# Kernel tuning notes

Measured on AMD Instinct MI355X. Metric: run time of the kernel, lower is better.

The kernel has to match this reference:

```python
import jax, jax.numpy as jnp
import numpy as np


def setup_inputs() -> dict:
    key = jax.random.key(0)
    k1, k2, k3, k4 = jax.random.split(key, 4)
    b, h, t, dim, topk = 16, 8, 196, 512, 49
    x = jax.random.normal(k1, (b, t, dim), dtype=jnp.float32)
    adj = jax.random.normal(k2, (b, h, t, t), dtype=jnp.float32)  # per-head routing logits
    Wqkv = jax.random.normal(k3, (dim, 3 * dim), dtype=jnp.float32) * 0.02
    Wv = jax.random.normal(k4, (dim, dim), dtype=jnp.float32) * 0.02
    return {"x": x, "adj": adj, "Wqkv": Wqkv, "Wv": Wv, "topk": topk}


def reference(x, adj, Wqkv, Wv, topk):
    b, t, dim = x.shape
    h = adj.shape[1]
    d = dim // h
    scale = dim ** (-0.5)  # note: full dim, matching source (self.scale = dim**-0.5)

    # qkv projection (stand-in for GIN conv_proj_qkv with nhid = 3*dim)
    qkv = (x @ Wqkv).reshape(b, t, h, 3 * d).transpose(0, 2, 1, 3)  # b h t 3d
    q, k, v = jnp.split(qkv, 3, axis=-1)  # each b h t d

    # TopkRouting: indices of top-k routing logits per (b, h, query-token)
    _, r_idx = jax.lax.top_k(adj, topk)  # b h t topk (r_weight unused: mul_weight='none')

    # KGather: irregular gather of concatenated k/v rows per query token
    kv = jnp.concatenate([k, v], axis=-1).reshape(b * h, t, 2 * d)
    idx = r_idx.reshape(b * h, t, topk)
    kv_sel = jax.vmap(lambda m, i: m[i])(kv, idx)          # (bh, t, topk, 2d)
    kv_sel = kv_sel.reshape(b, h, t, topk, 2 * d)
    k_sel, v_sel = jnp.split(kv_sel, 2, axis=-1)            # b h t topk d

    # small-window attention: each query attends to its topk gathered rows (w^2 = 1)
    attn = jax.nn.softmax(jnp.einsum('bhtd,bhtkd->bhtk', q * scale, k_sel), axis=-1)
    o = jnp.einsum('bhtk,bhtkd->bhtd', attn, v_sel)

    o = o.transpose(0, 2, 1, 3).reshape(b, t, dim)
    o = jax.nn.gelu(o, approximate=False)  # torch F.gelu default = exact erf
    return o @ Wv
```

## Files before the change

kernel.cpp:

```cpp
#include <hip/hip_runtime.h>
#include <hip/hip_bf16.h>
#include <cmath>

#define B_   16
#define H_   8
#define T_   196
#define DIM_ 512
#define DHEAD_ 64
#define TOPK_ 49
#define BT_  (B_ * T_)
#define BH_  (B_ * H_)

#define QB_OFF   0u
#define KB_OFF   1605632u
#define VT_OFF   3211264u
#define XB_OFF   5046272u
#define WQKVT_OFF 6651904u
#define WVT_OFF  7438336u
#define MASK_OFF 7700480u

#define QSPLIT_BLOCKS 3136

typedef __bf16 bf16x8 __attribute__((ext_vector_type(8)));
typedef float f32x4 __attribute__((ext_vector_type(4)));

__device__ __forceinline__ unsigned short f2bf(float f) {
    union { float f; unsigned int u; } v; v.f = f;
    const unsigned int u = v.u;
    return (unsigned short)((u + 0x7FFFu + ((u >> 16) & 1u)) >> 16);
}

__device__ __forceinline__ unsigned int ordered_u32(float f) {
    int i = __float_as_int(f);
    return (i < 0) ? ~(unsigned int)i : ((unsigned int)i | 0x80000000u);
}

__device__ __forceinline__ void gload16(const void* g, void* l) {
    __builtin_amdgcn_global_load_lds(
        (const __attribute__((address_space(1))) unsigned int*)g,
        (__attribute__((address_space(3))) unsigned int*)l, 16, 0, 0);
}

__device__ __forceinline__ void route_topk_q(const float* __restrict__ adj,
                                             unsigned int* __restrict__ masks,
                                             const int q, const int lane) {
    const float* arow = adj + (size_t)q * T_;
    const bool v3 = (lane < 4);
    unsigned int u[4];
    u[0] = ordered_u32(arow[lane]);
    u[1] = ordered_u32(arow[lane + 64]);
    u[2] = ordered_u32(arow[lane + 128]);
    u[3] = v3 ? ordered_u32(arow[lane + 192]) : 0u;

    unsigned int w0 = u[0], w1 = u[1], w2 = u[2], w3 = u[3];
    unsigned int prefix = 0u, thr = 0u;
    int k = TOPK_, A = T_;
    for (int b = 31; b >= 0; --b) {
        int C1 = 0;
        C1 += __popcll(__ballot((w0 >> b) == 1u));
        C1 += __popcll(__ballot((w1 >> b) == 1u));
        C1 += __popcll(__ballot((w2 >> b) == 1u));
        C1 += __popcll(__ballot((w3 >> b) == 1u));
        if (C1 >= k) {
            const unsigned int bit = 1u << b;
            prefix |= bit;
            w0 ^= bit; w1 ^= bit; w2 ^= bit; w3 ^= bit;
            A = C1;
        } else { k -= C1; A -= C1; }

        if (k == A || k == 1) {
            const bool mx = (k == 1);
            unsigned int best = mx ? 0u : 0xFFFFFFFFu;
            const unsigned int ww[4] = {w0, w1, w2, w3};
#pragma unroll
            for (int s2 = 0; s2 < 4; ++s2) {
                const bool valid = (s2 < 3) || v3;
                const bool act = valid && ((ww[s2] >> b) == 0u);
                if (act) best = mx ? (u[s2] > best ? u[s2] : best)
                                   : (u[s2] < best ? u[s2] : best);
            }
#pragma unroll
            for (int off = 32; off >= 1; off >>= 1) {
                const unsigned int o = __shfl_xor(best, off);
                best = mx ? (o > best ? o : best) : (o < best ? o : best);
            }
            thr = best;
            break;
        }
        if (b == 0) thr = prefix;
    }

    const unsigned long long lmask = (1ull << lane) - 1ull;
    unsigned long long gm[4];
    int G = 0;
#pragma unroll
    for (int s2 = 0; s2 < 4; ++s2) {
        const bool valid = (s2 < 3) || v3;
        gm[s2] = __ballot(valid && (u[s2] > thr));
        G += __popcll(gm[s2]);
    }
    const int need = TOPK_ - G;
    int cum = 0;
    unsigned long long sb0 = 0, sb1 = 0, sb2 = 0, sb3 = 0;
#pragma unroll
    for (int s2 = 0; s2 < 4; ++s2) {
        const bool valid = (s2 < 3) || v3;
        const bool e = valid && (u[s2] == thr);
        const unsigned long long em = __ballot(e);
        const int rk = cum + __popcll(em & lmask);
        cum += __popcll(em);
        const unsigned long long sel = gm[s2] | __ballot(e && (rk < need));
        if (s2 == 0) sb0 = sel; else if (s2 == 1) sb1 = sel;
        else if (s2 == 2) sb2 = sel; else sb3 = sel;
    }
    if (lane < 8) {
        const unsigned long long mv = (lane < 2) ? sb0 : (lane < 4) ? sb1
                                    : (lane < 6) ? sb2 : sb3;
        const unsigned int wd = (lane & 1) ? (unsigned int)(mv >> 32) : (unsigned int)mv;
        masks[(size_t)q * 8 + lane] = wd;
    }
}

__global__ __launch_bounds__(256) void prep(const float* __restrict__ x,
                                            const float* __restrict__ Wqkv,
                                            const float* __restrict__ Wv,
                                            const float* __restrict__ adj,
                                            unsigned short* __restrict__ xb,
                                            unsigned short* __restrict__ wqkvT,
                                            unsigned short* __restrict__ wvT,
                                            unsigned short* __restrict__ vT,
                                            unsigned int* __restrict__ masks) {
    __shared__ unsigned short Tt[64][72];
    const int t = threadIdx.x;
    const int bid = blockIdx.x;

    if (bid < QSPLIT_BLOCKS) {
        route_topk_q(adj, masks, bid * 4 + (t >> 6), t & 63);
        return;
    }
    int b2 = bid - QSPLIT_BLOCKS;
    if (b2 < 784) {
        const size_t base = ((size_t)b2 * 256 + t) * 8;
        const float4 v0 = *(const float4*)&x[base];
        const float4 v1 = *(const float4*)&x[base + 4];
        uint4 pk;
        pk.x = (unsigned int)f2bf(v0.x) | ((unsigned int)f2bf(v0.y) << 16);
        pk.y = (unsigned int)f2bf(v0.z) | ((unsigned int)f2bf(v0.w) << 16);
        pk.z = (unsigned int)f2bf(v1.x) | ((unsigned int)f2bf(v1.y) << 16);
        pk.w = (unsigned int)f2bf(v1.z) | ((unsigned int)f2bf(v1.w) << 16);
        *(uint4*)&xb[base] = pk;
        return;
    }
    b2 -= 784;
    if (b2 >= 192 && b2 < 220) {
        const int e0 = (b2 - 192) * 8192 + t;
#pragma unroll
        for (int i = 0; i < 32; ++i) {
            const int e = e0 + i * 256;
            const int bh = e / 1792;
            const int rem = e - bh * 1792;
            const int d = rem / 28;
            const int tt = rem - d * 28;
            vT[(size_t)bh * (64 * 224) + (size_t)d * 224 + 196 + tt] = 0;
        }
        return;
    }

    const float* src;
    unsigned short* dst;
    int Cc, tx, ty;
    if (b2 < 192) { src = Wqkv; dst = wqkvT; Cc = 1536; tx = b2 % 24; ty = b2 / 24; }
    else { const int b = b2 - 220; src = Wv; dst = wvT; Cc = 512; tx = b & 7; ty = b >> 3; }
    const int c0 = tx * 64, r0 = ty * 64;
#pragma unroll
    for (int p = 0; p < 4; ++p) {
        const int r = (t >> 4) + 16 * p;
        const int cl = (t & 15) * 4;
        const float4 v = *(const float4*)&src[(size_t)(r0 + r) * Cc + c0 + cl];
        Tt[cl + 0][r] = f2bf(v.x);
        Tt[cl + 1][r] = f2bf(v.y);
        Tt[cl + 2][r] = f2bf(v.z);
        Tt[cl + 3][r] = f2bf(v.w);
    }
    __syncthreads();
#pragma unroll
    for (int p = 0; p < 2; ++p) {
        const int cc = (t >> 3) + 32 * p;
        const int ch = (t & 7) * 8;
        *(uint4*)&dst[(size_t)(c0 + cc) * 512 + r0 + ch] = *(const uint4*)&Tt[cc][ch];
    }
}

template <int BN, int MODE, int FUSE, typename CT>
__global__ __launch_bounds__(256) void gemm_mfma(const unsigned short* __restrict__ A,
                                                 const unsigned short* __restrict__ Bt,
                                                 CT* __restrict__ C,
                                                 const int M, const int N, const int K,
                                                 const float* __restrict__ adj,
                                                 unsigned int* __restrict__ masks) {
    constexpr int FN = BN / 32;
    constexpr int CSZ = (MODE == 1) ? 64 * 132 : 1;
    struct ABt { unsigned short A[64][32]; unsigned short B[BN][32]; };
    __shared__ union {
        ABt ab[2];
        unsigned short Cs[CSZ];
    } sm;

    const int tid = threadIdx.x;
    const int lane = tid & 63, wid = tid >> 6;
    const int mt = M >> 6;
    const int nGemm = mt * (N / BN);
    const int bid = blockIdx.x;

    if constexpr (FUSE) {
        if (bid >= nGemm) {
            const int rid = bid - nGemm;
            route_topk_q(adj, masks, QSPLIT_BLOCKS * 4 + rid * 4 + wid, lane);
            return;
        }
    }

    const int bx = bid % mt;
    const int by = bid / mt;
    const int row0 = bx * 64;
    const int col0 = by * BN;
    const int wr = wid >> 1, wc = wid & 1;

    f32x4 acc[2][FN];
#pragma unroll
    for (int m = 0; m < 2; ++m)
#pragma unroll
        for (int n = 0; n < FN; ++n)
            acc[m][n] = (f32x4){0.0f, 0.0f, 0.0f, 0.0f};

    const int srow = lane >> 2;
    const int scol = (lane & 3) * 8;
    const unsigned short* aSrc = A + (size_t)(row0 + wid * 16 + srow) * K + scol;
    const unsigned short* bSrc = Bt + (size_t)(col0 + wid * 16 + srow) * K + scol;
    const unsigned short* bSrc2 = bSrc + (size_t)64 * K;

    const int fr = lane & 15;
    const int fk8 = (lane >> 4) * 8;

#define STAGE(BUF) do {                                                        \
        gload16(aSrc, &sm.ab[BUF].A[wid * 16][0]);                             \
        gload16(bSrc, &sm.ab[BUF].B[wid * 16][0]);                             \
        if constexpr (BN == 128) gload16(bSrc2, &sm.ab[BUF].B[64 + wid * 16][0]); \
        aSrc += 32; bSrc += 32; bSrc2 += 32;                                   \
    } while (0)

#define COMPUTE(BUF) do {                                                      \
        bf16x8 af[2], bfv[FN];                                                 \
        _Pragma("unroll")                                                      \
        for (int m = 0; m < 2; ++m)                                            \
            af[m] = *(const bf16x8*)&sm.ab[BUF].A[wr * 32 + m * 16 + fr][fk8]; \
        _Pragma("unroll")                                                      \
        for (int n = 0; n < FN; ++n)                                           \
            bfv[n] = *(const bf16x8*)&sm.ab[BUF].B[wc * (BN / 2) + n * 16 + fr][fk8]; \
        _Pragma("unroll")                                                      \
        for (int m = 0; m < 2; ++m)                                            \
            _Pragma("unroll")                                                  \
            for (int n = 0; n < FN; ++n)                                       \
                acc[m][n] = __builtin_amdgcn_mfma_f32_16x16x32_bf16(af[m], bfv[n], acc[m][n], 0, 0, 0); \
    } while (0)

    STAGE(0);
    __syncthreads();

    for (int k0 = 0; k0 < K; k0 += 64) {
        if (k0 + 32 < K) STAGE(1);
        COMPUTE(0);
        __syncthreads();
        if (k0 + 64 < K) STAGE(0);
        COMPUTE(1);
        __syncthreads();
    }
#undef STAGE
#undef COMPUTE

    if constexpr (MODE == 0) {
#pragma unroll
        for (int m = 0; m < 2; ++m)
#pragma unroll
            for (int n = 0; n < FN; ++n)
#pragma unroll
                for (int i = 0; i < 4; ++i) {
                    const int row = row0 + wr * 32 + m * 16 + (lane >> 4) * 4 + i;
                    const int col = col0 + wc * (BN / 2) + n * 16 + (lane & 15);
                    C[(size_t)row * N + col] = (CT)acc[m][n][i];
                }
    } else {
#pragma unroll
        for (int m = 0; m < 2; ++m)
#pragma unroll
            for (int n = 0; n < FN; ++n)
#pragma unroll
                for (int i = 0; i < 4; ++i) {
                    const int rl = wr * 32 + m * 16 + (lane >> 4) * 4 + i;
                    const int cl = wc * (BN / 2) + n * 16 + (lane & 15);
                    sm.Cs[rl * 132 + cl] = f2bf(acc[m][n][i]);
                }
        __syncthreads();

        unsigned short* ubase = (unsigned short*)C;
#pragma unroll
        for (int ch = 0; ch < BN / 64; ++ch) {
            const int abscol = col0 + ch * 64;
            const int which = (abscol >> 6) % 3;
            const int hh = abscol / 192;
            if (which < 2) {
                const int r = tid >> 2;
                const int co = (tid & 3) * 16;
                const int gr = row0 + r;
                const int bb = gr / T_;
                const int tt = gr - bb * T_;
                const uint2 a0 = *(const uint2*)&sm.Cs[r * 132 + ch * 64 + co];
                const uint2 a1 = *(const uint2*)&sm.Cs[r * 132 + ch * 64 + co + 4];
                const uint2 a2 = *(const uint2*)&sm.Cs[r * 132 + ch * 64 + co + 8];
                const uint2 a3 = *(const uint2*)&sm.Cs[r * 132 + ch * 64 + co + 12];
                unsigned short* dst = ubase + (size_t)which * KB_OFF +
                                      ((size_t)(bb * H_ + hh) * T_ + tt) * DHEAD_ + co;
                uint4 w0; w0.x = a0.x; w0.y = a0.y; w0.z = a1.x; w0.w = a1.y;
                uint4 w1; w1.x = a2.x; w1.y = a2.y; w1.z = a3.x; w1.w = a3.y;
                *(uint4*)&dst[0] = w0;
                *(uint4*)&dst[8] = w1;
            } else {
                const int d = tid >> 2;
                const int j0 = (tid & 3) * 16;
                union { unsigned short s[16]; uint2 v2[4]; } tmp;
#pragma unroll
                for (int j = 0; j < 16; ++j)
                    tmp.s[j] = sm.Cs[(j0 + j) * 132 + ch * 64 + d];
                const int gr0 = row0 + j0;
                const int bb0 = gr0 / T_;
                const int bb1 = (gr0 + 15) / T_;
                if (bb0 == bb1) {
                    const int tt = gr0 - bb0 * T_;
                    unsigned short* dst = ubase + VT_OFF +
                                          (size_t)(bb0 * H_ + hh) * (64 * 224) +
                                          (size_t)d * 224 + tt;
                    *(uint2*)&dst[0]  = tmp.v2[0];
                    *(uint2*)&dst[4]  = tmp.v2[1];
                    *(uint2*)&dst[8]  = tmp.v2[2];
                    *(uint2*)&dst[12] = tmp.v2[3];
                } else {
#pragma unroll
                    for (int j = 0; j < 16; ++j) {
                        const int gr = gr0 + j;
                        const int bb = gr / T_;
                        const int tt = gr - bb * T_;
                        ubase[VT_OFF + (size_t)(bb * H_ + hh) * (64 * 224) +
                              (size_t)d * 224 + tt] = tmp.s[j];
                    }
                }
            }
        }
    }
}

__global__ __launch_bounds__(64) void attn_mfma(const unsigned short* __restrict__ qb,
                                                const unsigned short* __restrict__ kb,
                                                const unsigned short* __restrict__ vT,
                                                const unsigned int* __restrict__ masks,
                                                unsigned short* __restrict__ obuf) {
    __shared__ unsigned int mask_lds[32][8];
    __shared__ unsigned short P[32][232];

    const int lane = threadIdx.x;
    const int qt = blockIdx.x;
    const int bh = blockIdx.y;
    const int bb = bh >> 3, hh = bh & 7;
    const int q0 = qt * 32;

#pragma unroll
    for (int p = 0; p < 4; ++p) {
        const int e = lane + p * 64;
        const int r = e >> 3, wd = e & 7;
        const int t = q0 + r;
        mask_lds[r][wd] = (t < T_) ? masks[((size_t)bh * T_ + t) * 8 + wd] : 0u;
    }
#pragma unroll
    for (int p = 0; p < 2; ++p) {
        const int e = lane + p * 64;
        if (e < 96) {
            const int r = e & 31, c8 = e >> 5;
            *(uint4*)&P[r][208 + c8 * 8] = (uint4){0u, 0u, 0u, 0u};
        }
    }
    __syncthreads();

    const int fr = lane & 15;
    const int fk8 = (lane >> 4) * 8;
    const unsigned short* qbh = qb + ((size_t)bh * T_ + q0) * DHEAD_;
    const unsigned short* kbh = kb + (size_t)bh * T_ * DHEAD_;

    const bf16x8 aq00 = *(const bf16x8*)&qbh[fr * 64 + fk8];
    const bf16x8 aq01 = *(const bf16x8*)&qbh[fr * 64 + 32 + fk8];
    const bf16x8 aq10 = *(const bf16x8*)&qbh[(16 + fr) * 64 + fk8];
    const bf16x8 aq11 = *(const bf16x8*)&qbh[(16 + fr) * 64 + 32 + fk8];

    f32x4 s0[13], s1[13];
#pragma unroll
    for (int c = 0; c < 13; ++c) {
        s0[c] = (f32x4){0.0f, 0.0f, 0.0f, 0.0f};
        s1[c] = (f32x4){0.0f, 0.0f, 0.0f, 0.0f};
    }
    __builtin_amdgcn_s_setprio(1);
#pragma unroll
    for (int c = 0; c < 13; ++c) {
        const bf16x8 b0 = *(const bf16x8*)&kbh[(c * 16 + fr) * 64 + fk8];
        const bf16x8 b1 = *(const bf16x8*)&kbh[(c * 16 + fr) * 64 + 32 + fk8];
        s0[c] = __builtin_amdgcn_mfma_f32_16x16x32_bf16(aq00, b0, s0[c], 0, 0, 0);
        s0[c] = __builtin_amdgcn_mfma_f32_16x16x32_bf16(aq01, b1, s0[c], 0, 0, 0);
        s1[c] = __builtin_amdgcn_mfma_f32_16x16x32_bf16(aq10, b0, s1[c], 0, 0, 0);
        s1[c] = __builtin_amdgcn_mfma_f32_16x16x32_bf16(aq11, b1, s1[c], 0, 0, 0);
    }
    __builtin_amdgcn_s_setprio(0);

    const float scale = 0.044194173824159216f;
    float lv[8];
#pragma unroll
    for (int tau = 0; tau < 2; ++tau)
#pragma unroll
        for (int i = 0; i < 4; ++i) {
            const int rowl = tau * 16 + (lane >> 4) * 4 + i;
            float li = 0.0f;
#pragma unroll
            for (int c = 0; c < 13; ++c) {
                const unsigned int mw = mask_lds[rowl][c >> 1];
                const bool sel = (mw >> (((c & 1) << 4) + fr)) & 1u;
                const float sv = (tau == 0) ? s0[c][i] : s1[c][i];
                const float pv = sel ? __expf(sv * scale) : 0.0f;
                P[rowl][c * 16 + fr] = f2bf(pv);
                li += pv;
            }
            lv[tau * 4 + i] = li;
        }
#pragma unroll
    for (int off = 8; off >= 1; off >>= 1)
#pragma unroll
        for (int j = 0; j < 8; ++j)
            lv[j] += __shfl_xor(lv[j], off);
    float rl[8];
#pragma unroll
    for (int j = 0; j < 8; ++j) rl[j] = 1.0f / lv[j];

    const unsigned short* vbh = vT + (size_t)bh * (64 * 224);
    f32x4 o0[4], o1[4];
#pragma unroll
    for (int n = 0; n < 4; ++n) {
        o0[n] = (f32x4){0.0f, 0.0f, 0.0f, 0.0f};
        o1[n] = (f32x4){0.0f, 0.0f, 0.0f, 0.0f};
    }
    __builtin_amdgcn_s_setprio(1);
#pragma unroll
    for (int kk = 0; kk < 7; ++kk) {
        const bf16x8 ap0 = *(const bf16x8*)&P[fr][kk * 32 + fk8];
        const bf16x8 ap1 = *(const bf16x8*)&P[16 + fr][kk * 32 + fk8];
#pragma unroll
        for (int n = 0; n < 4; ++n) {
            const bf16x8 bv = *(const bf16x8*)&vbh[(n * 16 + fr) * 224 + kk * 32 + fk8];
            o0[n] = __builtin_amdgcn_mfma_f32_16x16x32_bf16(ap0, bv, o0[n], 0, 0, 0);
            o1[n] = __builtin_amdgcn_mfma_f32_16x16x32_bf16(ap1, bv, o1[n], 0, 0, 0);
        }
    }
    __builtin_amdgcn_s_setprio(0);

#pragma unroll
    for (int tau = 0; tau < 2; ++tau)
#pragma unroll
        for (int i = 0; i < 4; ++i) {
            const float rli = rl[tau * 4 + i];
            const int t = q0 + tau * 16 + (lane >> 4) * 4 + i;
            if (t < T_) {
                unsigned short* orow = obuf + ((size_t)(bb * T_ + t)) * DIM_ + hh * DHEAD_;
#pragma unroll
                for (int n = 0; n < 4; ++n) {
                    const float ov = ((tau == 0) ? o0[n][i] : o1[n][i]) * rli;
                    const float g = 0.5f * ov * (1.0f + erff(ov * 0.70710678118654752f));
                    orow[n * 16 + fr] = f2bf(g);
                }
            }
        }
}

extern "C" void kernel_launch(void* const* d_in, const int* in_sizes, int n_in,
                              void* d_out, int out_size, void* d_ws, size_t ws_size,
                              hipStream_t stream) {
    const float* x    = (const float*)d_in[0];
    const float* adj  = (const float*)d_in[1];
    const float* Wqkv = (const float*)d_in[2];
    const float* Wv   = (const float*)d_in[3];
    float* out = (float*)d_out;
    unsigned short* ub = (unsigned short*)d_ws;

    unsigned short* qb    = ub + QB_OFF;
    unsigned short* kb    = ub + KB_OFF;
    unsigned short* vT    = ub + VT_OFF;
    unsigned short* xb    = ub + XB_OFF;
    unsigned short* wqkvT = ub + WQKVT_OFF;
    unsigned short* wvT   = ub + WVT_OFF;
    unsigned int*   masks = (unsigned int*)(ub + MASK_OFF);

    prep<<<4204, 256, 0, stream>>>(x, Wqkv, Wv, adj, xb, wqkvT, wvT, vT, masks);

    gemm_mfma<128, 1, 1, unsigned short><<<3724, 256, 0, stream>>>(
        xb, wqkvT, ub, BT_, 3 * DIM_, DIM_, adj, masks);

    attn_mfma<<<dim3(7, BH_), 64, 0, stream>>>(qb, kb, vT, masks, xb);

    gemm_mfma<64, 0, 0, float><<<392, 256, 0, stream>>>(
        xb, wvT, out, BT_, DIM_, DIM_, nullptr, nullptr);
}
```

Before: 67.54 us.

## Split attention keys across four waves with LDS reduction of partial outputs

```diff
diff --git a/kernel.cpp b/kernel.cpp
--- a/kernel.cpp
+++ b/kernel.cpp
@@ -358,130 +358,144 @@
     }
 }
 
-__global__ __launch_bounds__(64) void attn_mfma(const unsigned short* __restrict__ qb,
-                                                const unsigned short* __restrict__ kb,
-                                                const unsigned short* __restrict__ vT,
-                                                const unsigned int* __restrict__ masks,
-                                                unsigned short* __restrict__ obuf) {
-    __shared__ unsigned int mask_lds[32][8];
-    __shared__ unsigned short P[32][232];
-
-    const int lane = threadIdx.x;
+__global__ __launch_bounds__(256, 4) void attn_mfma(const unsigned short* __restrict__ qb,
+                                                    const unsigned short* __restrict__ kb,
+                                                    const unsigned short* __restrict__ vT,
+                                                    const unsigned int* __restrict__ masks,
+                                                    unsigned short* __restrict__ obuf) {
+    __shared__ union {
+        struct { unsigned int mask[16][8]; unsigned short P[4][16][72]; } p1;
+        struct { float Of[4][16][64]; float Lw[4][16]; } p2;
+    } sm;
+
+    const int tid = threadIdx.x;
+    const int lane = tid & 63;
+    const int w = tid >> 6;
     const int qt = blockIdx.x;
     const int bh = blockIdx.y;
     const int bb = bh >> 3, hh = bh & 7;
-    const int q0 = qt * 32;
-
-#pragma unroll
-    for (int p = 0; p < 4; ++p) {
-        const int e = lane + p * 64;
-        const int r = e >> 3, wd = e & 7;
+    const int q0 = qt * 16;
+
+    if (tid < 128) {
+        const int r = tid >> 3, wd = tid & 7;
         const int t = q0 + r;
-        mask_lds[r][wd] = (t < T_) ? masks[((size_t)bh * T_ + t) * 8 + wd] : 0u;
-    }
-#pragma unroll
-    for (int p = 0; p < 2; ++p) {
-        const int e = lane + p * 64;
-        if (e < 96) {
-            const int r = e & 31, c8 = e >> 5;
-            *(uint4*)&P[r][208 + c8 * 8] = (uint4){0u, 0u, 0u, 0u};
-        }
+        sm.p1.mask[r][wd] = (t < T_) ? masks[((size_t)bh * T_ + t) * 8 + wd] : 0u;
+    }
+    {
+        unsigned short* Pw = &sm.p1.P[w][0][0];
+        const int r = lane >> 2, c = (lane & 3) * 16;
+        *(uint4*)&Pw[r * 72 + c]     = (uint4){0u, 0u, 0u, 0u};
+        *(uint4*)&Pw[r * 72 + c + 8] = (uint4){0u, 0u, 0u, 0u};
     }
     __syncthreads();
 
     const int fr = lane & 15;
     const int fk8 = (lane >> 4) * 8;
+    const int nc = (w == 0) ? 4 : 3;
+    const int cbase = (w == 0) ? 0 : 1 + 3 * w;
+    const int keybase = cbase * 16;
+
     const unsigned short* qbh = qb + ((size_t)bh * T_ + q0) * DHEAD_;
     const unsigned short* kbh = kb + (size_t)bh * T_ * DHEAD_;
 
-    const bf16x8 aq00 = *(const bf16x8*)&qbh[fr * 64 + fk8];
-    const bf16x8 aq01 = *(const bf16x8*)&qbh[fr * 64 + 32 + fk8];
-    const bf16x8 aq10 = *(const bf16x8*)&qbh[(16 + fr) * 64 + fk8];
-    const bf16x8 aq11 = *(const bf16x8*)&qbh[(16 + fr) * 64 + 32 + fk8];
-
-    f32x4 s0[13], s1[13];
-#pragma unroll
-    for (int c = 0; c < 13; ++c) {
-        s0[c] = (f32x4){0.0f, 0.0f, 0.0f, 0.0f};
-        s1[c] = (f32x4){0.0f, 0.0f, 0.0f, 0.0f};
-    }
+    const bf16x8 aq0 = *(const bf16x8*)&qbh[fr * 64 + fk8];
+    const bf16x8 aq1 = *(const bf16x8*)&qbh[fr * 64 + 32 + fk8];
+
+    f32x4 s[4];
+#pragma unroll
+    for (int c2 = 0; c2 < 4; ++c2) s[c2] = (f32x4){0.0f, 0.0f, 0.0f, 0.0f};
     __builtin_amdgcn_s_setprio(1);
 #pragma unroll
-    for (int c = 0; c < 13; ++c) {
-        const bf16x8 b0 = *(const bf16x8*)&kbh[(c * 16 + fr) * 64 + fk8];
-        const bf16x8 b1 = *(const bf16x8*)&kbh[(c * 16 + fr) * 64 + 32 + fk8];
-        s0[c] = __builtin_amdgcn_mfma_f32_16x16x32_bf16(aq00, b0, s0[c], 0, 0, 0);
-        s0[c] = __builtin_amdgcn_mfma_f32_16x16x32_bf16(aq01, b1, s0[c], 0, 0, 0);
-        s1[c] = __builtin_amdgcn_mfma_f32_16x16x32_bf16(aq10, b0, s1[c], 0, 0, 0);
-        s1[c] = __builtin_amdgcn_mfma_f32_16x16x32_bf16(aq11, b1, s1[c], 0, 0, 0);
+    for (int c2 = 0; c2 < 4; ++c2) {
+        if (c2 < nc) {
+            const int c = cbase + c2;
+            const bf16x8 b0 = *(const bf16x8*)&kbh[(c * 16 + fr) * 64 + fk8];
+            const bf16x8 b1 = *(const bf16x8*)&kbh[(c * 16 + fr) * 64 + 32 + fk8];
+            s[c2] = __builtin_amdgcn_mfma_f32_16x16x32_bf16(aq0, b0, s[c2], 0, 0, 0);
+            s[c2] = __builtin_amdgcn_mfma_f32_16x16x32_bf16(aq1, b1, s[c2], 0, 0, 0);
+        }
     }
     __builtin_amdgcn_s_setprio(0);
 
     const float scale = 0.044194173824159216f;
-    float lv[8];
-#pragma unroll
-    for (int tau = 0; tau < 2; ++tau)
-#pragma unroll
-        for (int i = 0; i < 4; ++i) {
-            const int rowl = tau * 16 + (lane >> 4) * 4 + i;
-            float li = 0.0f;
-#pragma unroll
-            for (int c = 0; c < 13; ++c) {
-                const unsigned int mw = mask_lds[rowl][c >> 1];
+    float lv[4];
+#pragma unroll
+    for (int i = 0; i < 4; ++i) {
+        const int rowl = (lane >> 4) * 4 + i;
+        float li = 0.0f;
+#pragma unroll
+        for (int c2 = 0; c2 < 4; ++c2) {
+            if (c2 < nc) {
+                const int c = cbase + c2;
+                const unsigned int mw = sm.p1.mask[rowl][c >> 1];
                 const bool sel = (mw >> (((c & 1) << 4) + fr)) & 1u;
-                const float sv = (tau == 0) ? s0[c][i] : s1[c][i];
-                const float pv = sel ? __expf(sv * scale) : 0.0f;
-                P[rowl][c * 16 + fr] = f2bf(pv);
+                const float pv = sel ? __expf(s[c2][i] * scale) : 0.0f;
+                sm.p1.P[w][rowl][c2 * 16 + fr] = f2bf(pv);
                 li += pv;
             }
-            lv[tau * 4 + i] = li;
-        }
+        }
+        lv[i] = li;
+    }
 #pragma unroll
     for (int off = 8; off >= 1; off >>= 1)
 #pragma unroll
-        for (int j = 0; j < 8; ++j)
-            lv[j] += __shfl_xor(lv[j], off);
-    float rl[8];
-#pragma unroll
-    for (int j = 0; j < 8; ++j) rl[j] = 1.0f / lv[j];
-
-    const unsigned short* vbh = vT + (size_t)bh * (64 * 224);
-    f32x4 o0[4], o1[4];
+        for (int i = 0; i < 4; ++i)
+            lv[i] += __shfl_xor(lv[i], off);
+
+    const unsigned short* vbh = vT + (size_t)bh * (64 * 224) + keybase;
+    f32x4 o_p[4];
+#pragma unroll
+    for (int n = 0; n < 4; ++n) o_p[n] = (f32x4){0.0f, 0.0f, 0.0f, 0.0f};
+    const bf16x8 ap0 = *(const bf16x8*)&sm.p1.P[w][fr][fk8];
+    const bf16x8 ap1 = *(const bf16x8*)&sm.p1.P[w][fr][32 + fk8];
+    __builtin_amdgcn_s_setprio(1);
 #pragma unroll
     for (int n = 0; n < 4; ++n) {
-        o0[n] = (f32x4){0.0f, 0.0f, 0.0f, 0.0f};
-        o1[n] = (f32x4){0.0f, 0.0f, 0.0f, 0.0f};
-    }
-    __builtin_amdgcn_s_setprio(1);
-#pragma unroll
-    for (int kk = 0; kk < 7; ++kk) {
-        const bf16x8 ap0 = *(const bf16x8*)&P[fr][kk * 32 + fk8];
-        const bf16x8 ap1 = *(const bf16x8*)&P[16 + fr][kk * 32 + fk8];
-#pragma unroll
-        for (int n = 0; n < 4; ++n) {
-            const bf16x8 bv = *(const bf16x8*)&vbh[(n * 16 + fr) * 224 + kk * 32 + fk8];
-            o0[n] = __builtin_amdgcn_mfma_f32_16x16x32_bf16(ap0, bv, o0[n], 0, 0, 0);
-            o1[n] = __builtin_amdgcn_mfma_f32_16x16x32_bf16(ap1, bv, o1[n], 0, 0, 0);
-        }
+        const bf16x8 bv0 = *(const bf16x8*)&vbh[(n * 16 + fr) * 224 + fk8];
+        const bf16x8 bv1 = *(const bf16x8*)&vbh[(n * 16 + fr) * 224 + 32 + fk8];
+        o_p[n] = __builtin_amdgcn_mfma_f32_16x16x32_bf16(ap0, bv0, o_p[n], 0, 0, 0);
+        o_p[n] = __builtin_amdgcn_mfma_f32_16x16x32_bf16(ap1, bv1, o_p[n], 0, 0, 0);
     }
     __builtin_amdgcn_s_setprio(0);
 
-#pragma unroll
-    for (int tau = 0; tau < 2; ++tau)
-#pragma unroll
-        for (int i = 0; i < 4; ++i) {
-            const float rli = rl[tau * 4 + i];
-            const int t = q0 + tau * 16 + (lane >> 4) * 4 + i;
-            if (t < T_) {
-                unsigned short* orow = obuf + ((size_t)(bb * T_ + t)) * DIM_ + hh * DHEAD_;
-#pragma unroll
-                for (int n = 0; n < 4; ++n) {
-                    const float ov = ((tau == 0) ? o0[n][i] : o1[n][i]) * rli;
-                    const float g = 0.5f * ov * (1.0f + erff(ov * 0.70710678118654752f));
-                    orow[n * 16 + fr] = f2bf(g);
-                }
+    __syncthreads();
+
+#pragma unroll
+    for (int n = 0; n < 4; ++n)
+#pragma unroll
+        for (int i = 0; i < 4; ++i)
+            sm.p2.Of[w][(lane >> 4) * 4 + i][n * 16 + fr] = o_p[n][i];
+    if (fr == 0) {
+#pragma unroll
+        for (int i = 0; i < 4; ++i)
+            sm.p2.Lw[w][(lane >> 4) * 4 + i] = lv[i];
+    }
+    __syncthreads();
+
+    {
+        const int r = tid >> 4;
+        const int c0 = (tid & 15) * 4;
+        const int t = q0 + r;
+        if (t < T_) {
+            const float l = sm.p2.Lw[0][r] + sm.p2.Lw[1][r] +
+                            sm.p2.Lw[2][r] + sm.p2.Lw[3][r];
+            const float rl = 1.0f / l;
+            const f32x4 a0 = *(const f32x4*)&sm.p2.Of[0][r][c0];
+            const f32x4 a1 = *(const f32x4*)&sm.p2.Of[1][r][c0];
+            const f32x4 a2 = *(const f32x4*)&sm.p2.Of[2][r][c0];
+            const f32x4 a3 = *(const f32x4*)&sm.p2.Of[3][r][c0];
+            union { unsigned short s[4]; unsigned long long u; } pk;
+#pragma unroll
+            for (int j = 0; j < 4; ++j) {
+                const float ov = (a0[j] + a1[j] + a2[j] + a3[j]) * rl;
+                const float g = 0.5f * ov * (1.0f + erff(ov * 0.70710678118654752f));
+                pk.s[j] = f2bf(g);
             }
-        }
+            unsigned short* orow = obuf + ((size_t)(bb * T_ + t)) * DIM_ +
+                                   hh * DHEAD_ + c0;
+            *(unsigned long long*)orow = pk.u;
+        }
+    }
 }
 
 extern "C" void kernel_launch(void* const* d_in, const int* in_sizes, int n_in,
@@ -507,7 +521,7 @@
     gemm_mfma<128, 1, 1, unsigned short><<<3724, 256, 0, stream>>>(
         xb, wqkvT, ub, BT_, 3 * DIM_, DIM_, adj, masks);
 
-    attn_mfma<<<dim3(7, BH_), 64, 0, stream>>>(qb, kb, vT, masks, xb);
+    attn_mfma<<<dim3(13, BH_), 256, 0, stream>>>(qb, kb, vT, masks, xb);
 
     gemm_mfma<64, 0, 0, float><<<392, 256, 0, stream>>>(
         xb, wvT, out, BT_, DIM_, DIM_, nullptr, nullptr);
```

New measurement: 63.34 us. 1.07x faster.
